# Performance work log

Measured on AMD Instinct MI355X. Metric: run time of the kernel, lower is better.

The kernel has to match this reference:

```python
import jax, jax.numpy as jnp
import numpy as np
import math

B, T, C = 1, 2048, 2048
NH, HS = 16, 128          # hs = C // nh
NLQ, NLKV, DHR = 1536, 512, 64


def _rope(x, cos, sin):
    # x: [B, T, H, D]; cos/sin: [T, D//2]. Rotates pairs (even, odd) like
    # torch's complex-multiply apply_rotary_emb.
    xr = x.reshape(x.shape[:-1] + (-1, 2))
    x_re, x_im = xr[..., 0], xr[..., 1]
    c = cos[None, :, None, :]
    s = sin[None, :, None, :]
    out = jnp.stack([x_re * c - x_im * s, x_re * s + x_im * c], axis=-1)
    return out.reshape(x.shape)


def setup_inputs() -> dict:
    key = jax.random.key(0)
    ks = jax.random.split(key, 9)
    sc = 0.02  # init scale so logits stay sane
    x = jax.random.normal(ks[0], (B, T, C), jnp.float32)
    # RoPE tables (theta = 10000), matching precompute_freqs_cis
    inv = 1.0 / (10000.0 ** (jnp.arange(0, DHR, 2, dtype=jnp.float32) / DHR))
    ang = jnp.outer(jnp.arange(T, dtype=jnp.float32), inv)  # [T, DHR//2]
    return {
        "x": x,
        "freqs_cos": jnp.cos(ang),
        "freqs_sin": jnp.sin(ang),
        "W_dq": jax.random.normal(ks[1], (NLQ, C), jnp.float32) * sc,
        "W_uq": jax.random.normal(ks[2], (C, NLQ), jnp.float32) * sc,
        "W_dkv": jax.random.normal(ks[3], (NLKV, C), jnp.float32) * sc,
        "W_uk": jax.random.normal(ks[4], (C, NLKV), jnp.float32) * sc,
        "W_uv": jax.random.normal(ks[5], (C, NLKV), jnp.float32) * sc,
        "W_qr": jax.random.normal(ks[6], (NH * DHR, NLQ), jnp.float32) * sc,
        "W_kr": jax.random.normal(ks[7], (DHR, C), jnp.float32) * sc,
        "W_o": jax.random.normal(ks[8], (C, C), jnp.float32) * sc,
    }


def reference(x, freqs_cos, freqs_sin, W_dq, W_uq, W_dkv, W_uk, W_uv, W_qr, W_kr, W_o):
    # ---- low-rank query/kv down-projections ----
    c_q = x @ W_dq.T                       # [B,T,NLQ]
    c_kv = x @ W_dkv.T                     # [B,T,NLKV]  (no kv_cache: c_kv = new_c_kv)

    # ---- weight absorption (training path) ----
    # torch: W_uq.weight.view(1,nlq,nh,hs).transpose(1,2) @ W_uk.weight.view(1,nh,hs,nlkv)
    Wuq_h = W_uq.reshape(NLQ, NH, HS).transpose(1, 0, 2)   # [NH,NLQ,HS]
    Wuk_h = W_uk.reshape(NH, HS, NLKV)                     # [NH,HS,NLKV]
    k_eff = jnp.einsum('hql,hlk->hqk', Wuq_h, Wuk_h)       # [NH,NLQ,NLKV]
    # torch: (W_uv.weight.T @ W_o.weight.T).view(nlkv,nh,hs).transpose(0,1)
    v_eff = (W_uv.T @ W_o.T).reshape(NLKV, NH, HS).transpose(1, 0, 2)  # [NH,NLKV,HS]

    # ---- content attention scores in latent space ----
    attn_c = jnp.einsum('bhtk,bsk->bhts',
                        jnp.einsum('btq,hqk->bhtk', c_q, k_eff), c_kv)  # [B,NH,T,T]

    # ---- decoupled RoPE subspace ----
    k_r = _rope((x @ W_kr.T)[:, :, None, :], freqs_cos, freqs_sin)[:, :, 0, :]   # [B,T,DHR]
    q_r = _rope((c_q @ W_qr.T).reshape(B, T, NH, DHR), freqs_cos, freqs_sin)
    q_r = q_r.transpose(0, 2, 1, 3)                                              # [B,NH,T,DHR]
    attn_r = jnp.einsum('bhtd,bsd->bhts', q_r, k_r)                              # [B,NH,T,T]

    # ---- combine, causal mask, softmax ----
    scale = 1.0 / math.sqrt(HS + DHR)
    scores = (attn_c + attn_r) * scale
    causal = jnp.tril(jnp.ones((T, T), dtype=bool))  # mask = triu(diag=1) complement
    scores = jnp.where(causal[None, None], scores, jnp.float32(-jnp.inf))
    attn = jax.nn.softmax(scores, axis=-1)           # dropout p=0.0

    # ---- value path: attend in latent space, then absorbed up+output proj ----
    y_lat = jnp.einsum('bhts,bsk->bhtk', attn, c_kv)          # [B,NH,T,NLKV]
    y = jnp.einsum('bhtk,hkd->bhtd', y_lat, v_eff)            # [B,NH,T,HS]
    y = y.transpose(0, 2, 1, 3).reshape(B, T, C)              # [B,T,C] (W_o absorbed)
    return y
```

## Files before the change

kernel.cpp:

```cpp
#include <hip/hip_runtime.h>
#include <hip/hip_bf16.h>
#include <math.h>

typedef __bf16 bf16_t;
typedef __bf16 bf16x4 __attribute__((ext_vector_type(4)));
typedef __bf16 bf16x8 __attribute__((ext_vector_type(8)));
typedef float f32x4 __attribute__((ext_vector_type(4)));

#define T_DIM 2048
#define C_DIM 2048
#define NH 16
#define HS 128
#define NLQ 1536
#define NLKV 512
#define DHR 64
#define QKD 192

__constant__ int c_qt_tab[30] = {5,11,11,15,15,10,10,15,14,14,14,9,9,13,4,
                                 13,13,8,8,12,12,12,3,7,7,6,6,2,1,0};
__constant__ int c_pt_tab[30] = {0,0,1,0,1,0,1,2,0,1,2,0,1,0,0,
                                 1,2,0,1,0,1,2,0,0,1,0,1,0,0,0};
__constant__ int c_pbase[16]  = {0,0,0,0,0,0,0,2,4,6,8,10,12,15,18,21};

#define NSLOT_A 338

__device__ __forceinline__ int probe_f32(const bf16_t* __restrict__ x) {
  int lane = threadIdx.x & 63;
  int bad = 0;
#pragma unroll
  for (int i = 0; i < 4; ++i) {
    float v = (float)x[lane + i * 64];
    if (!(fabsf(v) < 1.0e6f)) bad = 1;
  }
  return (__ballot(bad) != 0ull) ? 1 : 0;
}

__device__ __forceinline__ float* opart_at(float* A, float* B, int pi) {
  return (pi < NSLOT_A) ? (A + (size_t)pi * 16384) : (B + (size_t)(pi - NSLOT_A) * 16384);
}
__device__ __forceinline__ const float* opart_atc(const float* A, const float* B, int pi) {
  return (pi < NSLOT_A) ? (A + (size_t)pi * 16384) : (B + (size_t)(pi - NSLOT_A) * 16384);
}

struct PrepPack {
  const void* src[9];
  bf16_t* dst[9];
  int n[9];
  const void* tsrc[2];
  bf16_t* tdst[2];
  int tR[2], tC[2], tbx[2];
};

__global__ __launch_bounds__(256) void prep_k(PrepPack p, const bf16_t* __restrict__ xprobe) {
  __shared__ bf16_t tile[32][33];
  const int f32 = probe_f32(xprobe);
  const int which = blockIdx.y;
  if (which < 9) {
    const int n = p.n[which];
    const int stride = gridDim.x * 256 * 8;
    for (int i = (blockIdx.x * 256 + threadIdx.x) * 8; i < n; i += stride) {
      if (f32) {
        const float* s = (const float*)p.src[which] + i;
        f32x4 lo = *(const f32x4*)s;
        f32x4 hi = *(const f32x4*)(s + 4);
        bf16x8 v;
#pragma unroll
        for (int j = 0; j < 4; ++j) { v[j] = (bf16_t)lo[j]; v[j + 4] = (bf16_t)hi[j]; }
        *(bf16x8*)(p.dst[which] + i) = v;
      } else {
        *(bf16x8*)(p.dst[which] + i) = *(const bf16x8*)((const bf16_t*)p.src[which] + i);
      }
    }
  } else {
    const int ts = which - 9;
    const int R = p.tR[ts], C = p.tC[ts], tbx = p.tbx[ts];
    const int ntiles = tbx * (R / 32);
    if ((int)blockIdx.x >= ntiles) return;
    const void* in = p.tsrc[ts];
    bf16_t* out = p.tdst[ts];
    int bx = (blockIdx.x % tbx) * 32, by = (blockIdx.x / tbx) * 32;
    int tx = threadIdx.x & 31, ty = threadIdx.x >> 5;
    for (int i = ty; i < 32; i += 8) {
      int r = by + i, c = bx + tx;
      size_t idx = (size_t)r * C + c;
      tile[i][tx] = f32 ? (bf16_t)((const float*)in)[idx] : ((const bf16_t*)in)[idx];
    }
    __syncthreads();
    for (int i = ty; i < 32; i += 8) {
      int r = bx + i, c = by + tx;
      out[(size_t)r * R + c] = tile[tx][i];
    }
  }
}

__device__ __forceinline__ void async16(const bf16_t* g, bf16_t* l) {
  __builtin_amdgcn_global_load_lds(
      (const __attribute__((address_space(1))) void*)g,
      (__attribute__((address_space(3))) void*)l, 16, 0, 0);
}

__device__ __forceinline__ float fexp2(float x) {
  return __builtin_amdgcn_exp2f(x);
}

#define BM 128
#define BN 128
#define BKG 64

struct GDesc {
  const bf16_t* A; const bf16_t* B; bf16_t* C;
  int M, N, K, lda, ldb, ldc, mb, bx0;
};
struct GGrp { GDesc d[3]; };

__global__ __launch_bounds__(256) void gemm_group(GGrp g, int nseg) {
  int bx = blockIdx.x;
  int s = 0;
  while (s + 1 < nseg && bx >= g.d[s + 1].bx0) ++s;
  const GDesc D = g.d[s];
  const int local = bx - D.bx0;
  const int bm = (local % D.mb) * BM, bn = (local / D.mb) * BN;

  __shared__ bf16_t As[2][BM * BKG];
  __shared__ bf16_t Bs[2][BN * BKG];
  const int tid = threadIdx.x;
  const int lane = tid & 63;
  const int wave = tid >> 6;
  const int l16 = lane & 15, quad = lane >> 4;
  const int wm = (wave >> 1) * 64, wn = (wave & 1) * 64;
  f32x4 acc[4][4] = {};

  const int nt = D.K / BKG;

#pragma unroll
  for (int r = 0; r < 4; ++r) {
    int c = r * 256 + tid;
    int row = c >> 3;
    int c8 = (c & 7) ^ (row & 7);
    int ar = bm + row; if (ar > D.M - 1) ar = D.M - 1;
    int br = bn + row; if (br > D.N - 1) br = D.N - 1;
    async16(D.A + (size_t)ar * D.lda + c8 * 8, &As[0][c * 8]);
    async16(D.B + (size_t)br * D.ldb + c8 * 8, &Bs[0][c * 8]);
  }
  asm volatile("s_waitcnt vmcnt(0)" ::: "memory");
  __builtin_amdgcn_s_barrier();

  for (int t = 0; t < nt; ++t) {
    const int cur = t & 1;
    if (t + 1 < nt) {
      const int k0 = (t + 1) * BKG;
#pragma unroll
      for (int r = 0; r < 4; ++r) {
        int c = r * 256 + tid;
        int row = c >> 3;
        int c8 = (c & 7) ^ (row & 7);
        int ar = bm + row; if (ar > D.M - 1) ar = D.M - 1;
        int br = bn + row; if (br > D.N - 1) br = D.N - 1;
        async16(D.A + (size_t)ar * D.lda + k0 + c8 * 8, &As[cur ^ 1][c * 8]);
        async16(D.B + (size_t)br * D.ldb + k0 + c8 * 8, &Bs[cur ^ 1][c * 8]);
      }
    }
#pragma unroll
    for (int kk = 0; kk < 2; ++kk) {
      bf16x8 af[4], bfr[4];
#pragma unroll
      for (int i = 0; i < 4; ++i) {
        int row = wm + i * 16 + l16;
        af[i] = *(const bf16x8*)(&As[cur][row * BKG + (((kk * 4 + quad) ^ (row & 7)) * 8)]);
      }
#pragma unroll
      for (int j = 0; j < 4; ++j) {
        int row = wn + j * 16 + l16;
        bfr[j] = *(const bf16x8*)(&Bs[cur][row * BKG + (((kk * 4 + quad) ^ (row & 7)) * 8)]);
      }
#pragma unroll
      for (int i = 0; i < 4; ++i)
#pragma unroll
        for (int j = 0; j < 4; ++j)
          acc[i][j] = __builtin_amdgcn_mfma_f32_16x16x32_bf16(af[i], bfr[j], acc[i][j], 0, 0, 0);
    }
    asm volatile("s_waitcnt vmcnt(0)" ::: "memory");
    __builtin_amdgcn_s_barrier();
  }

#pragma unroll
  for (int i = 0; i < 4; ++i)
#pragma unroll
    for (int j = 0; j < 4; ++j)
#pragma unroll
      for (int r = 0; r < 4; ++r) {
        int gm = bm + wm + i * 16 + quad * 4 + r;
        int gn = bn + wn + j * 16 + l16;
        if (gm < D.M && gn < D.N) D.C[(size_t)gm * D.ldc + gn] = (bf16_t)acc[i][j][r];
      }
}

__global__ void pack_qk_k(const bf16_t* __restrict__ qcat, const bf16_t* __restrict__ khead,
                          const bf16_t* __restrict__ xa,
                          const bf16_t* __restrict__ fc, const bf16_t* __restrict__ fs,
                          bf16_t* __restrict__ Qp, bf16_t* __restrict__ Kp) {
  int idx = blockIdx.x * blockDim.x + threadIdx.x;
  if (idx >= NH * T_DIM * 96) return;
  int j = idx % 96;
  int t = (idx / 96) % T_DIM;
  int h = idx / (96 * T_DIM);
  if (blockIdx.y == 0) {
    const float scale = 0.07216878364870323f;
    bf16_t* out = Qp + ((size_t)h * T_DIM + t) * QKD;
    if (j < 64) {
      float a = (float)qcat[(size_t)t * 3072 + h * HS + 2 * j];
      float b = (float)qcat[(size_t)t * 3072 + h * HS + 2 * j + 1];
      out[2 * j] = (bf16_t)(a * scale);
      out[2 * j + 1] = (bf16_t)(b * scale);
    } else {
      int i = j - 64;
      float re = (float)qcat[(size_t)t * 3072 + 2048 + h * DHR + 2 * i];
      float im = (float)qcat[(size_t)t * 3072 + 2048 + h * DHR + 2 * i + 1];
      float c = (float)fc[t * 32 + i], s = (float)fs[t * 32 + i];
      out[HS + 2 * i] = (bf16_t)((re * c - im * s) * scale);
      out[HS + 2 * i + 1] = (bf16_t)((re * s + im * c) * scale);
    }
  } else {
    bf16_t* out = Kp + ((size_t)h * T_DIM + t) * QKD;
    if (j < 64) {
      out[2 * j] = khead[(size_t)t * C_DIM + h * HS + 2 * j];
      out[2 * j + 1] = khead[(size_t)t * C_DIM + h * HS + 2 * j + 1];
    } else {
      int i = j - 64;
      float re = (float)xa[(size_t)t * 2112 + 2048 + 2 * i];
      float im = (float)xa[(size_t)t * 2112 + 2048 + 2 * i + 1];
      float c = (float)fc[t * 32 + i], s = (float)fs[t * 32 + i];
      out[HS + 2 * i] = (bf16_t)(re * c - im * s);
      out[HS + 2 * i + 1] = (bf16_t)(re * s + im * c);
    }
  }
}

#define FBM 128
#define FBN 64
#define KPITCH 200
#define VPITCH 72
#define PPITCH 72

__global__ __launch_bounds__(256) void flash_k(const bf16_t* __restrict__ Qp,
                                               const bf16_t* __restrict__ Kp,
                                               const bf16_t* __restrict__ VT,
                                               void* __restrict__ Y,
                                               const bf16_t* __restrict__ xprobe,
                                               float* __restrict__ OpartA,
                                               float* __restrict__ OpartB,
                                               float* __restrict__ Mpart,
                                               float* __restrict__ Lpart) {
  __shared__ bf16_t Ksm[FBN * KPITCH];
  __shared__ bf16_t Vtsm[HS * VPITCH];
  __shared__ bf16_t Psm[4][32 * PPITCH];
  const int tid = threadIdx.x;
  const int lane = tid & 63, wave = tid >> 6;
  const int l16 = lane & 15, quad = lane >> 4;
  const int id = blockIdx.x;
  const int xcd = id & 7, slot = id >> 3;
  const int h = xcd + 8 * (slot / 30);
  const int p = slot % 30;
  const int qt = c_qt_tab[p];
  const int part = c_pt_tab[p];
  const int nkv = 2 * qt + 2;
  const int nparts = (qt <= 5) ? 1 : (qt <= 11 ? 2 : 3);
  const int bse = nkv / nparts, rem = nkv % nparts;
  const int kt0 = part * bse + (part < rem ? part : rem);
  const int kt1 = kt0 + bse + (part < rem ? 1 : 0);
  const int partial = (nparts > 1);
  const int qb = qt * FBM;
  const int f32out = probe_f32(xprobe);
  const float L2E = 1.4426950408889634f;

  bf16x8 aq[2][6];
#pragma unroll
  for (int tt = 0; tt < 2; ++tt) {
    const bf16_t* qbase = Qp + ((size_t)h * T_DIM + qb + wave * 32 + tt * 16 + l16) * QKD;
#pragma unroll
    for (int c = 0; c < 6; ++c) aq[tt][c] = *(const bf16x8*)(qbase + c * 32 + quad * 8);
  }

  f32x4 o[2][8] = {};
  float m_i[2] = {-3.0e38f, -3.0e38f}, l_i[2] = {0.f, 0.f};

  const bf16_t* kg_base = Kp + (size_t)h * T_DIM * QKD;
  const bf16_t* vg_base = VT + (size_t)(h * HS) * T_DIM;

  bf16x8 kreg[6], vreg[4];
  {
    const bf16_t* kg = kg_base + (size_t)kt0 * FBN * QKD;
#pragma unroll
    for (int i = 0; i < 6; ++i) {
      int idx = i * 256 + tid;
      kreg[i] = *(const bf16x8*)(kg + (size_t)idx * 8);
    }
    const bf16_t* vg = vg_base + kt0 * FBN;
#pragma unroll
    for (int i = 0; i < 4; ++i) {
      int idx = i * 256 + tid, row = idx >> 3, c8 = idx & 7;
      vreg[i] = *(const bf16x8*)(vg + (size_t)row * T_DIM + c8 * 8);
    }
  }

  for (int kt = kt0; kt < kt1; ++kt) {
    __syncthreads();
#pragma unroll
    for (int i = 0; i < 6; ++i) {
      int idx = i * 256 + tid, row = idx / 24, c8 = idx % 24;
      *(bf16x8*)(Ksm + row * KPITCH + c8 * 8) = kreg[i];
    }
#pragma unroll
    for (int i = 0; i < 4; ++i) {
      int idx = i * 256 + tid, row = idx >> 3, c8 = idx & 7;
      *(bf16x8*)(Vtsm + row * VPITCH + c8 * 8) = vreg[i];
    }
    __syncthreads();
    if (kt + 1 < kt1) {
      const bf16_t* kg = kg_base + (size_t)(kt + 1) * FBN * QKD;
#pragma unroll
      for (int i = 0; i < 6; ++i) {
        int idx = i * 256 + tid;
        kreg[i] = *(const bf16x8*)(kg + (size_t)idx * 8);
      }
      const bf16_t* vg = vg_base + (kt + 1) * FBN;
#pragma unroll
      for (int i = 0; i < 4; ++i) {
        int idx = i * 256 + tid, row = idx >> 3, c8 = idx & 7;
        vreg[i] = *(const bf16x8*)(vg + (size_t)row * T_DIM + c8 * 8);
      }
    }
    f32x4 sc[2][4] = {};
#pragma unroll
    for (int nt = 0; nt < 4; ++nt)
#pragma unroll
      for (int c = 0; c < 6; ++c) {
        bf16x8 bk = *(const bf16x8*)(Ksm + (nt * 16 + l16) * KPITCH + c * 32 + quad * 8);
        sc[0][nt] = __builtin_amdgcn_mfma_f32_16x16x32_bf16(bk, aq[0][c], sc[0][nt], 0, 0, 0);
        sc[1][nt] = __builtin_amdgcn_mfma_f32_16x16x32_bf16(bk, aq[1][c], sc[1][nt], 0, 0, 0);
      }
    if (kt >= 2 * qt) {
#pragma unroll
      for (int tt = 0; tt < 2; ++tt) {
        int t_glob = qb + wave * 32 + tt * 16 + l16;
#pragma unroll
        for (int nt = 0; nt < 4; ++nt) {
          int s_base = kt * FBN + nt * 16 + quad * 4;
#pragma unroll
          for (int r = 0; r < 4; ++r)
            if (s_base + r > t_glob) sc[tt][nt][r] = -3.0e38f;
        }
      }
    }
#pragma unroll
    for (int tt = 0; tt < 2; ++tt) {
      float mx = sc[tt][0][0];
#pragma unroll
      for (int nt = 0; nt < 4; ++nt)
#pragma unroll
        for (int r = 0; r < 4; ++r) mx = fmaxf(mx, sc[tt][nt][r]);
      mx = fmaxf(mx, __shfl_xor(mx, 16, 64));
      mx = fmaxf(mx, __shfl_xor(mx, 32, 64));
      int need = (mx > m_i[tt] + 5.5f) ? 1 : 0;
      if (__any(need)) {
        float mn = fmaxf(m_i[tt], mx);
        float alpha = fexp2((m_i[tt] - mn) * L2E);
        m_i[tt] = mn;
        l_i[tt] *= alpha;
#pragma unroll
        for (int dt = 0; dt < 8; ++dt) o[tt][dt] *= alpha;
      }
      float rs = 0.f;
#pragma unroll
      for (int nt = 0; nt < 4; ++nt) {
        float p0 = fexp2((sc[tt][nt][0] - m_i[tt]) * L2E);
        float p1 = fexp2((sc[tt][nt][1] - m_i[tt]) * L2E);
        float p2 = fexp2((sc[tt][nt][2] - m_i[tt]) * L2E);
        float p3 = fexp2((sc[tt][nt][3] - m_i[tt]) * L2E);
        rs += (p0 + p1) + (p2 + p3);
        uint2 pk;
        asm("v_cvt_pk_bf16_f32 %0, %1, %2" : "=v"(pk.x) : "v"(p0), "v"(p1));
        asm("v_cvt_pk_bf16_f32 %0, %1, %2" : "=v"(pk.y) : "v"(p2), "v"(p3));
        *(uint2*)(&Psm[wave][(tt * 16 + l16) * PPITCH + nt * 16 + quad * 4]) = pk;
      }
      rs += __shfl_xor(rs, 16, 64);
      rs += __shfl_xor(rs, 32, 64);
      l_i[tt] += rs;
    }
#pragma unroll
    for (int s2 = 0; s2 < 2; ++s2) {
      bf16x8 ap0 = *(const bf16x8*)(&Psm[wave][l16 * PPITCH + s2 * 32 + quad * 8]);
      bf16x8 ap1 = *(const bf16x8*)(&Psm[wave][(16 + l16) * PPITCH + s2 * 32 + quad * 8]);
#pragma unroll
      for (int dt = 0; dt < 8; ++dt) {
        bf16x8 bv = *(const bf16x8*)(Vtsm + (dt * 16 + l16) * VPITCH + s2 * 32 + quad * 8);
        o[0][dt] = __builtin_amdgcn_mfma_f32_16x16x32_bf16(bv, ap0, o[0][dt], 0, 0, 0);
        o[1][dt] = __builtin_amdgcn_mfma_f32_16x16x32_bf16(bv, ap1, o[1][dt], 0, 0, 0);
      }
    }
  }

  if (!partial) {
#pragma unroll
    for (int tt = 0; tt < 2; ++tt) {
      float inv = 1.0f / l_i[tt];
      int t = qb + wave * 32 + tt * 16 + l16;
#pragma unroll
      for (int dt = 0; dt < 8; ++dt) {
        size_t oi = (size_t)t * C_DIM + h * HS + dt * 16 + quad * 4;
        if (f32out) {
          f32x4 v;
#pragma unroll
          for (int r = 0; r < 4; ++r) v[r] = o[tt][dt][r] * inv;
          *(f32x4*)((float*)Y + oi) = v;
        } else {
          bf16x4 v;
#pragma unroll
          for (int r = 0; r < 4; ++r) v[r] = (bf16_t)(o[tt][dt][r] * inv);
          *(bf16x4*)((bf16_t*)Y + oi) = v;
        }
      }
    }
  } else {
    const int pi = h * 24 + c_pbase[qt] + part;
    float* obase = opart_at(OpartA, OpartB, pi);
#pragma unroll
    for (int tt = 0; tt < 2; ++tt) {
      int rowl = wave * 32 + tt * 16 + l16;
      float* ob = obase + (size_t)rowl * 128;
#pragma unroll
      for (int dt = 0; dt < 8; ++dt) {
        f32x4 v = o[tt][dt];
        *(f32x4*)(ob + dt * 16 + quad * 4) = v;
      }
      if (quad == 0) {
        Mpart[(size_t)pi * 128 + rowl] = m_i[tt];
        Lpart[(size_t)pi * 128 + rowl] = l_i[tt];
      }
    }
  }
}

__global__ __launch_bounds__(256) void combine_k(const float* __restrict__ OpartA,
                                                 const float* __restrict__ OpartB,
                                                 const float* __restrict__ Mpart,
                                                 const float* __restrict__ Lpart,
                                                 void* __restrict__ Y,
                                                 const bf16_t* __restrict__ xprobe) {
  const int h = blockIdx.y;
  const int qt = 6 + blockIdx.x;
  const int c = (qt <= 11) ? 2 : 3;
  const int pib = h * 24 + c_pbase[qt];
  const int row = threadIdx.x >> 1;
  const int c0 = (threadIdx.x & 1) * 64;
  const int f32out = probe_f32(xprobe);
  const float L2E = 1.4426950408889634f;
  float m0 = Mpart[(size_t)pib * 128 + row];
  float m1 = Mpart[(size_t)(pib + 1) * 128 + row];
  float l0 = Lpart[(size_t)pib * 128 + row];
  float l1 = Lpart[(size_t)(pib + 1) * 128 + row];
  float m2 = -3.0e38f, l2 = 0.f;
  if (c == 3) {
    m2 = Mpart[(size_t)(pib + 2) * 128 + row];
    l2 = Lpart[(size_t)(pib + 2) * 128 + row];
  }
  float ms = fmaxf(m0, fmaxf(m1, m2));
  float w0 = fexp2((m0 - ms) * L2E);
  float w1 = fexp2((m1 - ms) * L2E);
  float w2 = fexp2((m2 - ms) * L2E);
  float inv = 1.0f / (l0 * w0 + l1 * w1 + l2 * w2);
  const float* O0 = opart_atc(OpartA, OpartB, pib) + (size_t)row * 128 + c0;
  const float* O1 = opart_atc(OpartA, OpartB, pib + 1) + (size_t)row * 128 + c0;
  const float* O2 = opart_atc(OpartA, OpartB, pib + 2) + (size_t)row * 128 + c0;
  int t = qt * 128 + row;
  size_t ob = (size_t)t * C_DIM + h * HS + c0;
#pragma unroll
  for (int d4 = 0; d4 < 64; d4 += 4) {
    f32x4 a = *(const f32x4*)(O0 + d4);
    f32x4 b = *(const f32x4*)(O1 + d4);
    f32x4 acc;
#pragma unroll
    for (int j = 0; j < 4; ++j) acc[j] = a[j] * w0 + b[j] * w1;
    if (c == 3) {
      f32x4 e = *(const f32x4*)(O2 + d4);
#pragma unroll
      for (int j = 0; j < 4; ++j) acc[j] += e[j] * w2;
    }
#pragma unroll
    for (int j = 0; j < 4; ++j) {
      float v = acc[j] * inv;
      if (f32out) ((float*)Y)[ob + d4 + j] = v;
      else        ((bf16_t*)Y)[ob + d4 + j] = (bf16_t)v;
    }
  }
}

extern "C" void kernel_launch(void* const* d_in, const int* in_sizes, int n_in,
                              void* d_out, int out_size, void* d_ws, size_t ws_size,
                              hipStream_t stream) {
  bf16_t* w = (bf16_t*)d_ws;
  const bf16_t* xprobe = (const bf16_t*)d_in[0];

  if (ws_size < (size_t)34472000 * 2 + 128) return;

  bf16_t* fcc    = w + 64;
  bf16_t* fsc    = w + 65600;
  bf16_t* xc     = w + 131136;
  bf16_t* BigB   = w + 4325440;
  bf16_t* dqc    = BigB;
  bf16_t* dkvc   = BigB + 3145728;
  bf16_t* krc    = BigB + 4194304;
  bf16_t* Bq     = w + 8650816;
  bf16_t* W_uq_t = Bq;
  bf16_t* qrc    = Bq + 3145728;
  bf16_t* xa     = w + 13369408;
  bf16_t* qcat   = w + 17694784;
  bf16_t* k_head = w + 23986240;
  bf16_t* vhatT  = w + 28180544;
  bf16_t* ukc    = w + 32374848;
  bf16_t* Pt     = w + 33423424;
  bf16_t* woc    = qcat;
  bf16_t* W_uv_t = k_head;
  bf16_t* Qpack  = xc;
  bf16_t* Kpack  = qcat;
  float* OpartA = (float*)(w + 6422592);
  float* Mpart  = (float*)(w + 17498176);
  float* Lpart  = (float*)(w + 17596480);
  float* OpartB = (float*)(w + 23986240);

  PrepPack pp;
  const void* srcs[9] = {d_in[1], d_in[2], d_in[0], d_in[3], d_in[5], d_in[9], d_in[8], d_in[6], d_in[10]};
  bf16_t* dsts[9]     = {fcc,     fsc,     xc,      dqc,     dkvc,    krc,     qrc,     ukc,     woc};
  int ns[9] = {T_DIM * 32, T_DIM * 32, T_DIM * C_DIM, NLQ * C_DIM, NLKV * C_DIM,
               DHR * C_DIM, NH * DHR * NLQ, C_DIM * NLKV, C_DIM * C_DIM};
  for (int i = 0; i < 9; ++i) { pp.src[i] = srcs[i]; pp.dst[i] = dsts[i]; pp.n[i] = ns[i]; }
  pp.tsrc[0] = d_in[4]; pp.tdst[0] = W_uq_t; pp.tR[0] = 1536; pp.tC[0] = 2048; pp.tbx[0] = 64;
  pp.tsrc[1] = d_in[7]; pp.tdst[1] = W_uv_t; pp.tR[1] = 2048; pp.tC[1] = 512;  pp.tbx[1] = 16;
  prep_k<<<dim3(3072, 11), 256, 0, stream>>>(pp, xprobe);

  {
    GGrp g;
    g.d[0] = {xc,  BigB,   xa, 2048, 2112, 2048, 2048, 2048, 2112, 16, 0};
    g.d[1] = {woc, W_uv_t, Pt, 2048,  512, 2048, 2048, 2048,  512, 16, 272};
    gemm_group<<<336, 256, 0, stream>>>(g, 2);
  }
  {
    GGrp g;
    g.d[0] = {xa,        Bq,        qcat,   2048, 3072, 1536, 2112, 1536, 3072, 16, 0};
    g.d[1] = {xa + 1536, ukc,       k_head, 2048, 2048,  512, 2112,  512, 2048, 16, 384};
    g.d[2] = {Pt,        xa + 1536, vhatT,  2048, 2048,  512,  512, 2112, 2048, 16, 640};
    gemm_group<<<896, 256, 0, stream>>>(g, 3);
  }

  int pk = (NH * T_DIM * 96 + 255) / 256;
  pack_qk_k<<<dim3(pk, 2), 256, 0, stream>>>(qcat, k_head, xa, fcc, fsc, Qpack, Kpack);

  flash_k<<<dim3(480), 256, 0, stream>>>(Qpack, Kpack, vhatT, d_out, xprobe,
                                         OpartA, OpartB, Mpart, Lpart);
  combine_k<<<dim3(10, NH), 256, 0, stream>>>(OpartA, OpartB, Mpart, Lpart, d_out, xprobe);
}
```

Measured before the change: 313.4 us.

## Use async global-to-LDS loads with XOR swizzle and shuffle-based P transfer in flash kernel

Replaces the register-staged K/V prefetch with direct async global-to-LDS copies into XOR-swizzled, unpadded shared buffers, waiting on vmcnt before compute. The P tile is now passed between lanes with cross-lane shuffles instead of a round trip through shared memory. It also adds s_setprio around the MFMA sections and sets launch bounds to 3 blocks per CU. The loss of overlap between the next tile's loads and current compute is meant to be covered by higher occupancy, but loads are now fully serialized within a block.

```diff
diff --git a/kernel.cpp b/kernel.cpp
--- a/kernel.cpp
+++ b/kernel.cpp
@@ -6,6 +6,7 @@
 typedef __bf16 bf16x4 __attribute__((ext_vector_type(4)));
 typedef __bf16 bf16x8 __attribute__((ext_vector_type(8)));
 typedef float f32x4 __attribute__((ext_vector_type(4)));
+typedef unsigned int u32x4 __attribute__((ext_vector_type(4)));
 
 #define T_DIM 2048
 #define C_DIM 2048
@@ -238,22 +239,18 @@
 
 #define FBM 128
 #define FBN 64
-#define KPITCH 200
-#define VPITCH 72
-#define PPITCH 72
-
-__global__ __launch_bounds__(256) void flash_k(const bf16_t* __restrict__ Qp,
-                                               const bf16_t* __restrict__ Kp,
-                                               const bf16_t* __restrict__ VT,
-                                               void* __restrict__ Y,
-                                               const bf16_t* __restrict__ xprobe,
-                                               float* __restrict__ OpartA,
-                                               float* __restrict__ OpartB,
-                                               float* __restrict__ Mpart,
-                                               float* __restrict__ Lpart) {
-  __shared__ bf16_t Ksm[FBN * KPITCH];
-  __shared__ bf16_t Vtsm[HS * VPITCH];
-  __shared__ bf16_t Psm[4][32 * PPITCH];
+
+__global__ __launch_bounds__(256, 3) void flash_k(const bf16_t* __restrict__ Qp,
+                                                  const bf16_t* __restrict__ Kp,
+                                                  const bf16_t* __restrict__ VT,
+                                                  void* __restrict__ Y,
+                                                  const bf16_t* __restrict__ xprobe,
+                                                  float* __restrict__ OpartA,
+                                                  float* __restrict__ OpartB,
+                                                  float* __restrict__ Mpart,
+                                                  float* __restrict__ Lpart) {
+  __shared__ bf16_t Ksm[FBN * 256];
+  __shared__ bf16_t Vtsm[HS * 64];
   const int tid = threadIdx.x;
   const int lane = tid & 63, wave = tid >> 6;
   const int l16 = lane & 15, quad = lane >> 4;
@@ -272,6 +269,10 @@
   const int qb = qt * FBM;
   const int f32out = probe_f32(xprobe);
   const float L2E = 1.4426950408889634f;
+  const int srcA = l16 + ((lane & 16) << 1);
+  const int srcB = srcA + 16;
+  const int hi = quad >> 1;
+  const int swz = l16 & 7;
 
   bf16x8 aq[2][6];
 #pragma unroll
@@ -287,58 +288,42 @@
   const bf16_t* kg_base = Kp + (size_t)h * T_DIM * QKD;
   const bf16_t* vg_base = VT + (size_t)(h * HS) * T_DIM;
 
-  bf16x8 kreg[6], vreg[4];
-  {
-    const bf16_t* kg = kg_base + (size_t)kt0 * FBN * QKD;
-#pragma unroll
-    for (int i = 0; i < 6; ++i) {
-      int idx = i * 256 + tid;
-      kreg[i] = *(const bf16x8*)(kg + (size_t)idx * 8);
-    }
-    const bf16_t* vg = vg_base + kt0 * FBN;
-#pragma unroll
-    for (int i = 0; i < 4; ++i) {
-      int idx = i * 256 + tid, row = idx >> 3, c8 = idx & 7;
-      vreg[i] = *(const bf16x8*)(vg + (size_t)row * T_DIM + c8 * 8);
-    }
-  }
-
   for (int kt = kt0; kt < kt1; ++kt) {
     __syncthreads();
-#pragma unroll
-    for (int i = 0; i < 6; ++i) {
-      int idx = i * 256 + tid, row = idx / 24, c8 = idx % 24;
-      *(bf16x8*)(Ksm + row * KPITCH + c8 * 8) = kreg[i];
-    }
+    const bf16_t* kg = kg_base + (size_t)kt * FBN * QKD;
+#pragma unroll
+    for (int i = 0; i < 8; ++i) {
+      int s = i * 256 + tid;
+      int row = s >> 5, gd = s & 31;
+      int gs = gd ^ (row & 7);
+      int off = (gs < 24) ? (row * QKD + gs * 8) : 0;
+      async16(kg + off, Ksm + s * 8);
+    }
+    const bf16_t* vg = vg_base + kt * FBN;
 #pragma unroll
     for (int i = 0; i < 4; ++i) {
-      int idx = i * 256 + tid, row = idx >> 3, c8 = idx & 7;
-      *(bf16x8*)(Vtsm + row * VPITCH + c8 * 8) = vreg[i];
-    }
+      int s = i * 256 + tid;
+      int row = s >> 3, gd = s & 7;
+      int gs = gd ^ (row & 7);
+      async16(vg + (size_t)row * T_DIM + gs * 8, Vtsm + s * 8);
+    }
+    asm volatile("s_waitcnt vmcnt(0)" ::: "memory");
     __syncthreads();
-    if (kt + 1 < kt1) {
-      const bf16_t* kg = kg_base + (size_t)(kt + 1) * FBN * QKD;
-#pragma unroll
-      for (int i = 0; i < 6; ++i) {
-        int idx = i * 256 + tid;
-        kreg[i] = *(const bf16x8*)(kg + (size_t)idx * 8);
-      }
-      const bf16_t* vg = vg_base + (kt + 1) * FBN;
-#pragma unroll
-      for (int i = 0; i < 4; ++i) {
-        int idx = i * 256 + tid, row = idx >> 3, c8 = idx & 7;
-        vreg[i] = *(const bf16x8*)(vg + (size_t)row * T_DIM + c8 * 8);
-      }
-    }
+
     f32x4 sc[2][4] = {};
-#pragma unroll
-    for (int nt = 0; nt < 4; ++nt)
+    __builtin_amdgcn_s_setprio(1);
+#pragma unroll
+    for (int nt = 0; nt < 4; ++nt) {
+      const bf16_t* krow = Ksm + (nt * 16 + l16) * 256;
 #pragma unroll
       for (int c = 0; c < 6; ++c) {
-        bf16x8 bk = *(const bf16x8*)(Ksm + (nt * 16 + l16) * KPITCH + c * 32 + quad * 8);
+        int gp = (c * 4 + quad) ^ swz;
+        bf16x8 bk = *(const bf16x8*)(krow + gp * 8);
         sc[0][nt] = __builtin_amdgcn_mfma_f32_16x16x32_bf16(bk, aq[0][c], sc[0][nt], 0, 0, 0);
         sc[1][nt] = __builtin_amdgcn_mfma_f32_16x16x32_bf16(bk, aq[1][c], sc[1][nt], 0, 0, 0);
       }
+    }
+    __builtin_amdgcn_s_setprio(0);
     if (kt >= 2 * qt) {
 #pragma unroll
       for (int tt = 0; tt < 2; ++tt) {
@@ -352,6 +337,7 @@
         }
       }
     }
+    unsigned int pk32[2][4][2];
 #pragma unroll
     for (int tt = 0; tt < 2; ++tt) {
       float mx = sc[tt][0][0];
@@ -378,26 +364,44 @@
         float p2 = fexp2((sc[tt][nt][2] - m_i[tt]) * L2E);
         float p3 = fexp2((sc[tt][nt][3] - m_i[tt]) * L2E);
         rs += (p0 + p1) + (p2 + p3);
-        uint2 pk;
-        asm("v_cvt_pk_bf16_f32 %0, %1, %2" : "=v"(pk.x) : "v"(p0), "v"(p1));
-        asm("v_cvt_pk_bf16_f32 %0, %1, %2" : "=v"(pk.y) : "v"(p2), "v"(p3));
-        *(uint2*)(&Psm[wave][(tt * 16 + l16) * PPITCH + nt * 16 + quad * 4]) = pk;
+        asm("v_cvt_pk_bf16_f32 %0, %1, %2" : "=v"(pk32[tt][nt][0]) : "v"(p0), "v"(p1));
+        asm("v_cvt_pk_bf16_f32 %0, %1, %2" : "=v"(pk32[tt][nt][1]) : "v"(p2), "v"(p3));
       }
       rs += __shfl_xor(rs, 16, 64);
       rs += __shfl_xor(rs, 32, 64);
       l_i[tt] += rs;
     }
+    __builtin_amdgcn_s_setprio(1);
 #pragma unroll
     for (int s2 = 0; s2 < 2; ++s2) {
-      bf16x8 ap0 = *(const bf16x8*)(&Psm[wave][l16 * PPITCH + s2 * 32 + quad * 8]);
-      bf16x8 ap1 = *(const bf16x8*)(&Psm[wave][(16 + l16) * PPITCH + s2 * 32 + quad * 8]);
+      u32x4 wa, wb;
+#pragma unroll
+      for (int c = 0; c < 2; ++c) {
+        unsigned int a0 = (unsigned int)__shfl((int)pk32[0][2 * s2][c], srcA, 64);
+        unsigned int a1 = (unsigned int)__shfl((int)pk32[0][2 * s2 + 1][c], srcA, 64);
+        wa[c] = hi ? a1 : a0;
+        unsigned int a2 = (unsigned int)__shfl((int)pk32[0][2 * s2][c], srcB, 64);
+        unsigned int a3 = (unsigned int)__shfl((int)pk32[0][2 * s2 + 1][c], srcB, 64);
+        wa[2 + c] = hi ? a3 : a2;
+        unsigned int b0 = (unsigned int)__shfl((int)pk32[1][2 * s2][c], srcA, 64);
+        unsigned int b1 = (unsigned int)__shfl((int)pk32[1][2 * s2 + 1][c], srcA, 64);
+        wb[c] = hi ? b1 : b0;
+        unsigned int b2 = (unsigned int)__shfl((int)pk32[1][2 * s2][c], srcB, 64);
+        unsigned int b3 = (unsigned int)__shfl((int)pk32[1][2 * s2 + 1][c], srcB, 64);
+        wb[2 + c] = hi ? b3 : b2;
+      }
+      bf16x8 ap0 = __builtin_bit_cast(bf16x8, wa);
+      bf16x8 ap1 = __builtin_bit_cast(bf16x8, wb);
 #pragma unroll
       for (int dt = 0; dt < 8; ++dt) {
-        bf16x8 bv = *(const bf16x8*)(Vtsm + (dt * 16 + l16) * VPITCH + s2 * 32 + quad * 8);
+        int row = dt * 16 + l16;
+        int gp = (s2 * 4 + quad) ^ swz;
+        bf16x8 bv = *(const bf16x8*)(Vtsm + row * 64 + gp * 8);
         o[0][dt] = __builtin_amdgcn_mfma_f32_16x16x32_bf16(bv, ap0, o[0][dt], 0, 0, 0);
         o[1][dt] = __builtin_amdgcn_mfma_f32_16x16x32_bf16(bv, ap1, o[1][dt], 0, 0, 0);
       }
     }
+    __builtin_amdgcn_s_setprio(0);
   }
 
   if (!partial) {
```

Result: slower. 364.1 us (+16.2%).

## Replace LDS P staging with cross-lane shuffles, add setprio and occupancy hint

Applied to the files above, without the earlier changes.

The softmax probability tile no longer goes through a per-wave shared-memory buffer. The packed bf16 values are redistributed into the MFMA operand layout with ds_bpermute-style shuffles and selects, which frees LDS and removes the store/load round trip. The MFMA sections are wrapped in s_setprio to favour matrix issue, and launch_bounds now requests 3 blocks per CU. The cost is extra shuffle instructions and more register pressure under the tighter occupancy bound, which could cause spills.

```diff
diff --git a/kernel.cpp b/kernel.cpp
--- a/kernel.cpp
+++ b/kernel.cpp
@@ -6,6 +6,7 @@
 typedef __bf16 bf16x4 __attribute__((ext_vector_type(4)));
 typedef __bf16 bf16x8 __attribute__((ext_vector_type(8)));
 typedef float f32x4 __attribute__((ext_vector_type(4)));
+typedef unsigned int u32x4 __attribute__((ext_vector_type(4)));
 
 #define T_DIM 2048
 #define C_DIM 2048
@@ -240,20 +241,18 @@
 #define FBN 64
 #define KPITCH 200
 #define VPITCH 72
-#define PPITCH 72
-
-__global__ __launch_bounds__(256) void flash_k(const bf16_t* __restrict__ Qp,
-                                               const bf16_t* __restrict__ Kp,
-                                               const bf16_t* __restrict__ VT,
-                                               void* __restrict__ Y,
-                                               const bf16_t* __restrict__ xprobe,
-                                               float* __restrict__ OpartA,
-                                               float* __restrict__ OpartB,
-                                               float* __restrict__ Mpart,
-                                               float* __restrict__ Lpart) {
+
+__global__ __launch_bounds__(256, 3) void flash_k(const bf16_t* __restrict__ Qp,
+                                                  const bf16_t* __restrict__ Kp,
+                                                  const bf16_t* __restrict__ VT,
+                                                  void* __restrict__ Y,
+                                                  const bf16_t* __restrict__ xprobe,
+                                                  float* __restrict__ OpartA,
+                                                  float* __restrict__ OpartB,
+                                                  float* __restrict__ Mpart,
+                                                  float* __restrict__ Lpart) {
   __shared__ bf16_t Ksm[FBN * KPITCH];
   __shared__ bf16_t Vtsm[HS * VPITCH];
-  __shared__ bf16_t Psm[4][32 * PPITCH];
   const int tid = threadIdx.x;
   const int lane = tid & 63, wave = tid >> 6;
   const int l16 = lane & 15, quad = lane >> 4;
@@ -272,6 +271,9 @@
   const int qb = qt * FBM;
   const int f32out = probe_f32(xprobe);
   const float L2E = 1.4426950408889634f;
+  const int srcA = l16 + ((lane & 16) << 1);
+  const int srcB = srcA + 16;
+  const int hi = quad >> 1;
 
   bf16x8 aq[2][6];
 #pragma unroll
@@ -331,6 +333,7 @@
       }
     }
     f32x4 sc[2][4] = {};
+    __builtin_amdgcn_s_setprio(1);
 #pragma unroll
     for (int nt = 0; nt < 4; ++nt)
 #pragma unroll
@@ -339,6 +342,7 @@
         sc[0][nt] = __builtin_amdgcn_mfma_f32_16x16x32_bf16(bk, aq[0][c], sc[0][nt], 0, 0, 0);
         sc[1][nt] = __builtin_amdgcn_mfma_f32_16x16x32_bf16(bk, aq[1][c], sc[1][nt], 0, 0, 0);
       }
+    __builtin_amdgcn_s_setprio(0);
     if (kt >= 2 * qt) {
 #pragma unroll
       for (int tt = 0; tt < 2; ++tt) {
@@ -352,6 +356,7 @@
         }
       }
     }
+    unsigned int pk32[2][4][2];
 #pragma unroll
     for (int tt = 0; tt < 2; ++tt) {
       float mx = sc[tt][0][0];
@@ -378,19 +383,34 @@
         float p2 = fexp2((sc[tt][nt][2] - m_i[tt]) * L2E);
         float p3 = fexp2((sc[tt][nt][3] - m_i[tt]) * L2E);
         rs += (p0 + p1) + (p2 + p3);
-        uint2 pk;
-        asm("v_cvt_pk_bf16_f32 %0, %1, %2" : "=v"(pk.x) : "v"(p0), "v"(p1));
-        asm("v_cvt_pk_bf16_f32 %0, %1, %2" : "=v"(pk.y) : "v"(p2), "v"(p3));
-        *(uint2*)(&Psm[wave][(tt * 16 + l16) * PPITCH + nt * 16 + quad * 4]) = pk;
+        asm("v_cvt_pk_bf16_f32 %0, %1, %2" : "=v"(pk32[tt][nt][0]) : "v"(p0), "v"(p1));
+        asm("v_cvt_pk_bf16_f32 %0, %1, %2" : "=v"(pk32[tt][nt][1]) : "v"(p2), "v"(p3));
       }
       rs += __shfl_xor(rs, 16, 64);
       rs += __shfl_xor(rs, 32, 64);
       l_i[tt] += rs;
     }
+    __builtin_amdgcn_s_setprio(1);
 #pragma unroll
     for (int s2 = 0; s2 < 2; ++s2) {
-      bf16x8 ap0 = *(const bf16x8*)(&Psm[wave][l16 * PPITCH + s2 * 32 + quad * 8]);
-      bf16x8 ap1 = *(const bf16x8*)(&Psm[wave][(16 + l16) * PPITCH + s2 * 32 + quad * 8]);
+      u32x4 wa, wb;
+#pragma unroll
+      for (int c = 0; c < 2; ++c) {
+        unsigned int a0 = (unsigned int)__shfl((int)pk32[0][2 * s2][c], srcA, 64);
+        unsigned int a1 = (unsigned int)__shfl((int)pk32[0][2 * s2 + 1][c], srcA, 64);
+        wa[c] = hi ? a1 : a0;
+        unsigned int a2 = (unsigned int)__shfl((int)pk32[0][2 * s2][c], srcB, 64);
+        unsigned int a3 = (unsigned int)__shfl((int)pk32[0][2 * s2 + 1][c], srcB, 64);
+        wa[2 + c] = hi ? a3 : a2;
+        unsigned int b0 = (unsigned int)__shfl((int)pk32[1][2 * s2][c], srcA, 64);
+        unsigned int b1 = (unsigned int)__shfl((int)pk32[1][2 * s2 + 1][c], srcA, 64);
+        wb[c] = hi ? b1 : b0;
+        unsigned int b2 = (unsigned int)__shfl((int)pk32[1][2 * s2][c], srcB, 64);
+        unsigned int b3 = (unsigned int)__shfl((int)pk32[1][2 * s2 + 1][c], srcB, 64);
+        wb[2 + c] = hi ? b3 : b2;
+      }
+      bf16x8 ap0 = __builtin_bit_cast(bf16x8, wa);
+      bf16x8 ap1 = __builtin_bit_cast(bf16x8, wb);
 #pragma unroll
       for (int dt = 0; dt < 8; ++dt) {
         bf16x8 bv = *(const bf16x8*)(Vtsm + (dt * 16 + l16) * VPITCH + s2 * 32 + quad * 8);
@@ -398,6 +418,7 @@
         o[1][dt] = __builtin_amdgcn_mfma_f32_16x16x32_bf16(bv, ap1, o[1][dt], 0, 0, 0);
       }
     }
+    __builtin_amdgcn_s_setprio(0);
   }
 
   if (!partial) {
```

Result: slower. 410.9 us (+31.1%).
